# Performance work log

Measured on AMD Instinct MI355X. Metric: run time of the kernel, lower is better.

## Reference

```python
import jax, jax.numpy as jnp
import numpy as np

B, N, D, H, K, MSL = 16, 512, 512, 8, 16, 512
HD = D // H
EPS = 1e-5


def _ln(x, g, b):
    m = jnp.mean(x, axis=-1, keepdims=True)
    v = jnp.mean((x - m) ** 2, axis=-1, keepdims=True)
    return (x - m) * jax.lax.rsqrt(v + EPS) * g + b


def setup_inputs() -> dict:
    key = jax.random.key(0)
    ks = jax.random.split(key, 12)
    s = 0.02
    d = {
        'x': jax.random.normal(ks[0], (B, N, D), jnp.float32),
        'wq': jax.random.normal(ks[1], (D, D), jnp.float32) * s,
        'bq': jnp.zeros((D,), jnp.float32),
        'wk': jax.random.normal(ks[2], (D, D), jnp.float32) * s,
        'bk': jnp.zeros((D,), jnp.float32),
        'wv': jax.random.normal(ks[3], (D, D), jnp.float32) * s,
        'bv': jnp.zeros((D,), jnp.float32),
        'wo': jax.random.normal(ks[4], (D, D), jnp.float32) * s,
        'bo': jnp.zeros((D,), jnp.float32),
        'g1': jnp.ones((D,), jnp.float32),
        'be1': jnp.zeros((D,), jnp.float32),
        'g2': jnp.ones((D,), jnp.float32),
        'be2': jnp.zeros((D,), jnp.float32),
        'w1': jax.random.normal(ks[5], (D, 4 * D), jnp.float32) * s,
        'bf1': jnp.zeros((4 * D,), jnp.float32),
        'w2': jax.random.normal(ks[6], (4 * D, D), jnp.float32) * s,
        'bf2': jnp.zeros((D,), jnp.float32),
        'rel_emb': jax.random.normal(ks[7], (2 * MSL - 1, H), jnp.float32) * s,
    }
    return d


def reference(x, wq, bq, wk, bk, wv, bv, wo, bo, g1, be1, g2, be2, w1, bf1, w2, bf2, rel_emb):
    # Pre-norm attention (dropout = identity, eval mode)
    xn = _ln(x, g1, be1)
    Q = (xn @ wq + bq).reshape(B, N, H, HD)
    Kh = (xn @ wk + bk).reshape(B, N, H, HD)
    V = (xn @ wv + bv).reshape(B, N, H, HD)
    scale = HD ** -0.5
    logits = jnp.einsum('bnhd,bmhd->bhnm', Q, Kh) * scale  # (B,H,N,N)
    # relative temporal bias
    pos = jnp.arange(N)
    drel = pos[None, :] - pos[:, None] + (MSL - 1)  # (N,N)
    bias = rel_emb[drel]  # (N,N,H)
    logits = logits + jnp.transpose(bias, (2, 0, 1))[None]
    # top-k sparsification + softmax over surviving entries only
    vals, idx = jax.lax.top_k(logits, K)  # (B,H,N,K)
    attn_k = jax.nn.softmax(vals, axis=-1)  # softmax over -inf-masked row == softmax over top-k
    # scatter probabilities back into dense (B,H,N,N) rows
    rows = jnp.zeros((B * H * N, N), logits.dtype)
    attn = jax.vmap(lambda r, i, v: r.at[i].set(v))(
        rows, idx.reshape(-1, K), attn_k.reshape(-1, K)
    ).reshape(B, H, N, N)
    out = jnp.einsum('bhnm,bmhd->bnhd', attn, V).reshape(B, N, D)
    out = out @ wo + bo
    x = x + out
    # feed-forward (GELU exact, matching torch default)
    xn2 = _ln(x, g2, be2)
    ff = jax.nn.gelu(xn2 @ w1 + bf1, approximate=False) @ w2 + bf2
    return x + ff
```

## Files before the change

### kernel.cpp

```cpp
#include <hip/hip_runtime.h>
#include <hip/hip_bf16.h>

#define BB 16
#define NN 512
#define DD 512
#define HH 8
#define HD 64
#define MM (BB*NN)
#define DFF 2048

typedef __attribute__((ext_vector_type(8))) short bf16x8;
typedef __attribute__((ext_vector_type(4))) float fx4;

static __device__ __forceinline__ unsigned short f2bf(float f) {
  unsigned u = __float_as_uint(f);
  u += 0x7FFFu + ((u >> 16) & 1u);
  return (unsigned short)(u >> 16);
}
static __device__ __forceinline__ float bf2f(unsigned short s) {
  return __uint_as_float(((unsigned)s) << 16);
}

static __device__ __forceinline__ void load_lds16(const unsigned short* g, unsigned short* l) {
  __builtin_amdgcn_global_load_lds(
      (const __attribute__((address_space(1))) void*)g,
      (__attribute__((address_space(3))) void*)l, 16, 0, 0);
}

__global__ void transpose_all(const float* __restrict__ wq, const float* __restrict__ wk,
                              const float* __restrict__ wv, const float* __restrict__ wo,
                              const float* __restrict__ w1, const float* __restrict__ w2,
                              unsigned short* __restrict__ wqkvT, unsigned short* __restrict__ woT,
                              unsigned short* __restrict__ w1T, unsigned short* __restrict__ w2T) {
  __shared__ float tl[32][33];
  int id = blockIdx.x;
  const float* src; unsigned short* dst; int K, N, bx, by;
  if (id < 1024) {
    int m = id >> 8, tt = id & 255;
    src = (m == 0) ? wq : (m == 1) ? wk : (m == 2) ? wv : wo;
    dst = (m == 3) ? woT : wqkvT + m * 512 * 512;
    K = 512; N = 512; bx = tt & 15; by = tt >> 4;
  } else if (id < 2048) {
    int tt = id - 1024;
    src = w1; dst = w1T; K = 512; N = 2048; bx = tt & 63; by = tt >> 6;
  } else {
    int tt = id - 2048;
    src = w2; dst = w2T; K = 2048; N = 512; bx = tt & 15; by = tt >> 4;
  }
  int tx = threadIdx.x, ty = threadIdx.y;
  int x0 = bx * 32, y0 = by * 32;
  #pragma unroll
  for (int i = 0; i < 4; i++)
    tl[ty + i*8][tx] = src[(size_t)(y0 + ty + i*8) * N + x0 + tx];
  __syncthreads();
  #pragma unroll
  for (int i = 0; i < 4; i++)
    dst[(size_t)(x0 + ty + i*8) * K + y0 + tx] = f2bf(tl[tx][ty + i*8]);
}

__global__ void concat_bias(const float* __restrict__ bq, const float* __restrict__ bk,
                            const float* __restrict__ bv, float* __restrict__ o) {
  int t = blockIdx.x * 256 + threadIdx.x;
  if (t < 512) o[t] = bq[t];
  else if (t < 1024) o[t] = bk[t - 512];
  else if (t < 1536) o[t] = bv[t - 1024];
}

__global__ __launch_bounds__(256) void ln_kernel(const float* __restrict__ X,
                                                 const float* __restrict__ g,
                                                 const float* __restrict__ be,
                                                 unsigned short* __restrict__ O) {
  int w = threadIdx.x >> 6, l = threadIdx.x & 63;
  size_t row = (size_t)blockIdx.x * 4 + w;
  const float* xr = X + row * 512;
  fx4 a = *(const fx4*)(xr + l*4);
  fx4 c = *(const fx4*)(xr + 256 + l*4);
  float s = a[0]+a[1]+a[2]+a[3] + c[0]+c[1]+c[2]+c[3];
  float q = a[0]*a[0]+a[1]*a[1]+a[2]*a[2]+a[3]*a[3]
          + c[0]*c[0]+c[1]*c[1]+c[2]*c[2]+c[3]*c[3];
  #pragma unroll
  for (int s2 = 1; s2 < 64; s2 <<= 1) { s += __shfl_xor(s, s2); q += __shfl_xor(q, s2); }
  float mean = s * (1.0f/512.0f);
  float var  = q * (1.0f/512.0f) - mean*mean;
  float rs = rsqrtf(var + 1e-5f);
  fx4 ga = *(const fx4*)(g + l*4);
  fx4 gc = *(const fx4*)(g + 256 + l*4);
  fx4 ba = *(const fx4*)(be + l*4);
  fx4 bc = *(const fx4*)(be + 256 + l*4);
  ushort4 o1, o2;
  o1.x = f2bf((a[0]-mean)*rs*ga[0] + ba[0]);
  o1.y = f2bf((a[1]-mean)*rs*ga[1] + ba[1]);
  o1.z = f2bf((a[2]-mean)*rs*ga[2] + ba[2]);
  o1.w = f2bf((a[3]-mean)*rs*ga[3] + ba[3]);
  o2.x = f2bf((c[0]-mean)*rs*gc[0] + bc[0]);
  o2.y = f2bf((c[1]-mean)*rs*gc[1] + bc[1]);
  o2.z = f2bf((c[2]-mean)*rs*gc[2] + bc[2]);
  o2.w = f2bf((c[3]-mean)*rs*gc[3] + bc[3]);
  *(ushort4*)(O + row*512 + l*4) = o1;
  *(ushort4*)(O + row*512 + 256 + l*4) = o2;
}

template<int MODE, int TN>
__global__ __launch_bounds__(256) void gemm_kernel(
    const unsigned short* __restrict__ A,
    const unsigned short* __restrict__ Bm,
    const float* __restrict__ bias,
    const float* resid,
    void* C,
    int M, int N, int K) {
  constexpr int MI  = (TN == 128) ? 2 : 1;
  constexpr int BW  = (TN == 128) ? 32 : 16;
  constexpr int NBI = (TN == 128) ? 4 : 2;
  __shared__ unsigned short As[64*64];
  __shared__ unsigned short Bs[TN*64];
  int m0 = blockIdx.y * 64, n0 = blockIdx.x * TN;
  int t = threadIdx.x;
  int w = t >> 6, l = t & 63;
  int wm = (TN == 128) ? (w >> 1) : w;
  int wn = (TN == 128) ? (w & 1) : 0;
  int lid = l & 15, quad = l >> 4;
  int lrow = l >> 3, lch = (l & 7) ^ lrow;

  const unsigned short* gA = A  + (size_t)(m0 + w*16 + lrow)*K + lch*8;
  const unsigned short* gB = Bm + (size_t)(n0 + w*BW + lrow)*K + lch*8;
  unsigned short* lA0 = As + (w*16    )*64;
  unsigned short* lA1 = As + (w*16 + 8)*64;
  unsigned short* lB[NBI];
  #pragma unroll
  for (int i = 0; i < NBI; i++) lB[i] = Bs + (w*BW + i*8)*64;

  fx4 acc[MI][4];
  #pragma unroll
  for (int i = 0; i < MI; i++)
    #pragma unroll
    for (int j = 0; j < 4; j++) acc[i][j] = (fx4){0.f,0.f,0.f,0.f};

  int xA = (lid & 7) * 8;

  for (int k0 = 0; k0 < K; k0 += 64) {
    load_lds16(gA,       lA0);
    load_lds16(gA + 8*K, lA1);
    #pragma unroll
    for (int i = 0; i < NBI; i++) load_lds16(gB + (size_t)(i*8)*K, lB[i]);
    gA += 64; gB += 64;
    __syncthreads();
    #pragma unroll
    for (int s = 0; s < 2; s++) {
      int cbase = (s*4 + quad) * 8;
      bf16x8 af[MI], bf[4];
      #pragma unroll
      for (int i = 0; i < MI; i++) {
        int ra = wm*(MI*16) + i*16 + lid;
        af[i] = *(const bf16x8*)(As + ra*64 + (cbase ^ xA));
      }
      #pragma unroll
      for (int j = 0; j < 4; j++) {
        int rb = wn*64 + j*16 + lid;
        bf[j] = *(const bf16x8*)(Bs + rb*64 + (cbase ^ xA));
      }
      #pragma unroll
      for (int i = 0; i < MI; i++)
        #pragma unroll
        for (int j = 0; j < 4; j++)
          acc[i][j] = __builtin_amdgcn_mfma_f32_16x16x32_bf16(af[i], bf[j], acc[i][j], 0, 0, 0);
    }
    __syncthreads();
  }

  #pragma unroll
  for (int i = 0; i < MI; i++) {
    #pragma unroll
    for (int j = 0; j < 4; j++) {
      int col = n0 + wn*64 + j*16 + lid;
      float bv = bias[col];
      #pragma unroll
      for (int r = 0; r < 4; r++) {
        int row = m0 + wm*(MI*16) + i*16 + quad*4 + r;
        float v = acc[i][j][r] + bv;
        if (MODE == 0) {
          if (col < 512) v *= 0.125f;
          ((unsigned short*)C)[(size_t)row*N + col] = f2bf(v);
        } else if (MODE == 1 || MODE == 3) {
          v += resid[(size_t)row*N + col];
          ((float*)C)[(size_t)row*N + col] = v;
        } else {
          float gl = 0.5f * v * (1.0f + erff(v * 0.70710678118654752f));
          ((unsigned short*)C)[(size_t)row*N + col] = f2bf(gl);
        }
      }
    }
  }
}

__global__ __launch_bounds__(256) void attn_kernel(
    const unsigned short* __restrict__ QKV,
    const float* __restrict__ rel_emb,
    unsigned short* __restrict__ Aout) {
  __shared__ float smem[6144];
  unsigned short* Ks = (unsigned short*)smem;
  float* bias_s = smem + 4608;
  float* pr = smem + 5632;
  int blk = blockIdx.x;
  int q0 = (blk & 7) << 6;
  int bh = blk >> 3;
  int b = bh >> 3, h = bh & 7;
  int t = threadIdx.x;
  int w = t >> 6, l = t & 63;
  int lid = l & 15, quad = l >> 4;

  for (int i = t; i < 1023; i += 256) bias_s[i] = rel_emb[i*8 + h];

  int qn = q0 + w*16 + lid;
  const unsigned short* qp = QKV + ((size_t)(b*512 + qn))*1536 + h*64 + quad*8;
  bf16x8 qf0 = *(const bf16x8*)qp;
  bf16x8 qf1 = *(const bf16x8*)(qp + 32);

  fx4 acc[32];
  #pragma unroll
  for (int i = 0; i < 32; i++) acc[i] = (fx4){0.f,0.f,0.f,0.f};

  #pragma unroll
  for (int chunk = 0; chunk < 4; chunk++) {
    __syncthreads();
    #pragma unroll
    for (int i = 0; i < 4; i++) {
      int c = t + i*256;
      int row = c >> 3, ch = c & 7;
      uint4 d = *(const uint4*)(QKV + ((size_t)(b*512 + chunk*128 + row))*1536 + 512 + h*64 + ch*8);
      *(uint4*)(Ks + row*72 + ch*8) = d;
    }
    __syncthreads();
    #pragma unroll
    for (int kt = 0; kt < 8; kt++) {
      const unsigned short* kp = Ks + (kt*16 + lid)*72 + quad*8;
      bf16x8 kb0 = *(const bf16x8*)kp;
      bf16x8 kb1 = *(const bf16x8*)(kp + 32);
      int ai = chunk*8 + kt;
      acc[ai] = __builtin_amdgcn_mfma_f32_16x16x32_bf16(qf0, kb0, acc[ai], 0, 0, 0);
      acc[ai] = __builtin_amdgcn_mfma_f32_16x16x32_bf16(qf1, kb1, acc[ai], 0, 0, 0);
    }
  }

  int nb = q0 + w*16 + quad*4;
  #pragma unroll
  for (int kt = 0; kt < 32; kt++) {
    int m = kt*16 + lid;
    int bidx = m - nb + 511;
    #pragma unroll
    for (int r = 0; r < 4; r++) {
      float v = acc[kt][r] + bias_s[bidx - r];
      unsigned mu = __float_as_uint(v);
      mu = (mu & 0x80000000u) ? ~mu : (mu | 0x80000000u);
      acc[kt][r] = __uint_as_float((mu & 0xFFFFFE00u) | (unsigned)(511 - m));
    }
  }

  unsigned mx0=0, mx1=0, mx2=0, mx3=0;
  #pragma unroll
  for (int kt = 0; kt < 32; kt++) {
    unsigned u0 = __float_as_uint(acc[kt][0]); mx0 = u0 > mx0 ? u0 : mx0;
    unsigned u1 = __float_as_uint(acc[kt][1]); mx1 = u1 > mx1 ? u1 : mx1;
    unsigned u2 = __float_as_uint(acc[kt][2]); mx2 = u2 > mx2 ? u2 : mx2;
    unsigned u3 = __float_as_uint(acc[kt][3]); mx3 = u3 > mx3 ? u3 : mx3;
  }
  unsigned mn0=mx0, mn1=mx1, mn2=mx2, mn3=mx3;
  #pragma unroll
  for (int s2 = 1; s2 < 16; s2 <<= 1) {
    unsigned o;
    o = __shfl_xor(mn0, s2); mn0 = o < mn0 ? o : mn0;
    o = __shfl_xor(mn1, s2); mn1 = o < mn1 ? o : mn1;
    o = __shfl_xor(mn2, s2); mn2 = o < mn2 ? o : mn2;
    o = __shfl_xor(mn3, s2); mn3 = o < mn3 ? o : mn3;
    o = __shfl_xor(mx0, s2); mx0 = o > mx0 ? o : mx0;
    o = __shfl_xor(mx1, s2); mx1 = o > mx1 ? o : mx1;
    o = __shfl_xor(mx2, s2); mx2 = o > mx2 ? o : mx2;
    o = __shfl_xor(mx3, s2); mx3 = o > mx3 ? o : mx3;
  }
  unsigned lo0 = mn0 - (mn0 ? 1u : 0u), hi0 = mx0;
  unsigned lo1 = mn1 - (mn1 ? 1u : 0u), hi1 = mx1;
  unsigned lo2 = mn2 - (mn2 ? 1u : 0u), hi2 = mx2;
  unsigned lo3 = mn3 - (mn3 ? 1u : 0u), hi3 = mx3;

  unsigned th0=0, th1=0, th2=0, th3=0;
  unsigned done = 0;
  #pragma unroll 1
  for (int it = 0; it < 34; ++it) {
    unsigned d_;
    d_ = hi0-lo0; unsigned mid0 = lo0 + (d_>>1) + (d_&1u);
    d_ = hi1-lo1; unsigned mid1 = lo1 + (d_>>1) + (d_&1u);
    d_ = hi2-lo2; unsigned mid2 = lo2 + (d_>>1) + (d_&1u);
    d_ = hi3-lo3; unsigned mid3 = lo3 + (d_>>1) + (d_&1u);
    unsigned c0=0, c1=0, c2=0, c3=0;
    #pragma unroll
    for (int kt = 0; kt < 32; kt++) {
      c0 += (__float_as_uint(acc[kt][0]) >= mid0);
      c1 += (__float_as_uint(acc[kt][1]) >= mid1);
      c2 += (__float_as_uint(acc[kt][2]) >= mid2);
      c3 += (__float_as_uint(acc[kt][3]) >= mid3);
    }
    unsigned p01 = c0 | (c1 << 16);
    unsigned p23 = c2 | (c3 << 16);
    #pragma unroll
    for (int s2 = 1; s2 < 16; s2 <<= 1) {
      p01 += __shfl_xor(p01, s2);
      p23 += __shfl_xor(p23, s2);
    }
    unsigned C0 = p01 & 0xFFFFu, C1 = p01 >> 16;
    unsigned C2 = p23 & 0xFFFFu, C3 = p23 >> 16;
    { bool f = !(done & 1u); bool e = f && (C0 == 16u);
      th0 = e ? mid0 : th0; done |= e ? 1u : 0u;
      lo0 = (f && C0 > 16u) ? mid0 : lo0; hi0 = (f && C0 < 16u) ? mid0 : hi0; }
    { bool f = !(done & 2u); bool e = f && (C1 == 16u);
      th1 = e ? mid1 : th1; done |= e ? 2u : 0u;
      lo1 = (f && C1 > 16u) ? mid1 : lo1; hi1 = (f && C1 < 16u) ? mid1 : hi1; }
    { bool f = !(done & 4u); bool e = f && (C2 == 16u);
      th2 = e ? mid2 : th2; done |= e ? 4u : 0u;
      lo2 = (f && C2 > 16u) ? mid2 : lo2; hi2 = (f && C2 < 16u) ? mid2 : hi2; }
    { bool f = !(done & 8u); bool e = f && (C3 == 16u);
      th3 = e ? mid3 : th3; done |= e ? 8u : 0u;
      lo3 = (f && C3 > 16u) ? mid3 : lo3; hi3 = (f && C3 < 16u) ? mid3 : hi3; }
    if (__all((int)(done == 15u))) break;
  }

  float* prE = pr + w*128 + quad*32;
  int*   prM = (int*)prE + 16;
  unsigned below = (1u << lid) - 1u;
  #pragma unroll
  for (int r = 0; r < 4; r++) {
    unsigned thr = (r==0) ? th0 : (r==1) ? th1 : (r==2) ? th2 : th3;
    int base = 0;
    #pragma unroll
    for (int kt = 0; kt < 32; kt++) {
      unsigned u = __float_as_uint(acc[kt][r]);
      bool sel = u >= thr;
      unsigned long long bm = __ballot(sel);
      unsigned gm = (unsigned)(bm >> (quad*16)) & 0xFFFFu;
      if (sel) {
        int slot = base + __popc(gm & below);
        unsigned vu = u & 0xFFFFFE00u;
        vu = (vu & 0x80000000u) ? (vu & 0x7FFFFFFFu) : ~vu;
        float e = exp2f(__uint_as_float(vu) * 1.44269504f);
        if (slot < 16) { prE[slot] = e; prM[slot] = 511 - (int)(u & 0x1FFu); }
      }
      base += __popc(gm);
    }
    __threadfence_block();
    int n = nb + r;
    float o0=0.f, o1=0.f, o2=0.f, o3=0.f, es=0.f;
    #pragma unroll
    for (int k2 = 0; k2 < 16; k2++) {
      float e = prE[k2];
      int m = prM[k2];
      const unsigned short* vp = QKV + ((size_t)(b*512 + m))*1536 + 1024 + h*64 + lid*4;
      ushort4 v4 = *(const ushort4*)vp;
      es += e;
      o0 += e * bf2f(v4.x); o1 += e * bf2f(v4.y);
      o2 += e * bf2f(v4.z); o3 += e * bf2f(v4.w);
    }
    float inv = 1.0f / es;
    ushort4 ov;
    ov.x = f2bf(o0*inv); ov.y = f2bf(o1*inv);
    ov.z = f2bf(o2*inv); ov.w = f2bf(o3*inv);
    *(ushort4*)(Aout + ((size_t)(b*512 + n))*512 + h*64 + lid*4) = ov;
    __threadfence_block();
  }
}

extern "C" void kernel_launch(void* const* d_in, const int* in_sizes, int n_in,
                              void* d_out, int out_size, void* d_ws, size_t ws_size,
                              hipStream_t stream) {
  const float* x   = (const float*)d_in[0];
  const float* wq  = (const float*)d_in[1];
  const float* bq  = (const float*)d_in[2];
  const float* wk  = (const float*)d_in[3];
  const float* bk  = (const float*)d_in[4];
  const float* wv  = (const float*)d_in[5];
  const float* bv  = (const float*)d_in[6];
  const float* wo  = (const float*)d_in[7];
  const float* bo  = (const float*)d_in[8];
  const float* g1  = (const float*)d_in[9];
  const float* be1 = (const float*)d_in[10];
  const float* g2  = (const float*)d_in[11];
  const float* be2 = (const float*)d_in[12];
  const float* w1  = (const float*)d_in[13];
  const float* bf1 = (const float*)d_in[14];
  const float* w2  = (const float*)d_in[15];
  const float* bf2 = (const float*)d_in[16];
  const float* rel = (const float*)d_in[17];

  char* p = (char*)d_ws;
  size_t off = 0;
  auto alloc = [&](size_t bytes) {
    size_t cur = off;
    off += (bytes + 255) & ~(size_t)255;
    return (void*)(p + cur);
  };
  unsigned short* wqkvT = (unsigned short*)alloc((size_t)1536*512*2);
  unsigned short* woT   = (unsigned short*)alloc((size_t)512*512*2);
  unsigned short* w1T   = (unsigned short*)alloc((size_t)2048*512*2);
  unsigned short* w2T   = (unsigned short*)alloc((size_t)512*2048*2);
  float*          bqkv  = (float*)alloc(1536*4);
  unsigned short* R1    = (unsigned short*)alloc((size_t)MM*512*2);
  unsigned short* R2    = (unsigned short*)alloc((size_t)MM*2048*2);

  unsigned short* xn1  = R1;
  unsigned short* aout = R1;
  unsigned short* xn2  = R1;
  unsigned short* qkvb = R2;
  unsigned short* hbuf = R2;
  float*          x2   = (float*)d_out;
  (void)ws_size; (void)in_sizes; (void)n_in; (void)out_size;

  transpose_all<<<3072, dim3(32, 8), 0, stream>>>(wq, wk, wv, wo, w1, w2,
                                                  wqkvT, woT, w1T, w2T);
  concat_bias<<<6, 256, 0, stream>>>(bq, bk, bv, bqkv);

  ln_kernel<<<2048, 256, 0, stream>>>(x, g1, be1, xn1);
  gemm_kernel<0,128><<<dim3(12, 128), 256, 0, stream>>>(xn1, wqkvT, bqkv, nullptr, qkvb, MM, 1536, 512);
  attn_kernel<<<1024, 256, 0, stream>>>(qkvb, rel, aout);
  gemm_kernel<1,64><<<dim3(8, 128), 256, 0, stream>>>(aout, woT, bo, x, x2, MM, 512, 512);
  ln_kernel<<<2048, 256, 0, stream>>>(x2, g2, be2, xn2);
  gemm_kernel<2,128><<<dim3(16, 128), 256, 0, stream>>>(xn2, w1T, bf1, nullptr, hbuf, MM, 2048, 512);
  gemm_kernel<3,64><<<dim3(8, 128), 256, 0, stream>>>(hbuf, w2T, bf2, x2, (float*)d_out, MM, 512, 2048);
}
```

Baseline: 347.3 us.

## Double-buffer K tiles via async global-to-LDS loads with XOR swizzle

The attention kernel now stages K chunks into two LDS buffers using direct global-to-LDS loads, prefetching the next chunk while MFMAs consume the current one, which halves the barriers per chunk. The padded layout is replaced by an XOR-swizzled 64-wide layout to avoid bank conflicts without padding. The top-k probability scratch is also double-buffered by row parity so a trailing fence can be dropped. LDS use grows from 24KB to 40KB, which may lower occupancy, and correctness depends on load_lds16 completing before the barrier.

```diff
diff --git a/kernel.cpp b/kernel.cpp
--- a/kernel.cpp
+++ b/kernel.cpp
@@ -196,10 +196,11 @@
     const unsigned short* __restrict__ QKV,
     const float* __restrict__ rel_emb,
     unsigned short* __restrict__ Aout) {
-  __shared__ float smem[6144];
-  unsigned short* Ks = (unsigned short*)smem;
-  float* bias_s = smem + 4608;
-  float* pr = smem + 5632;
+  __shared__ float smem[10240];
+  unsigned short* K0 = (unsigned short*)smem;
+  unsigned short* K1 = (unsigned short*)(smem + 4096);
+  float* bias_s = smem + 8192;
+  float* pr = smem + 9216;
   int blk = blockIdx.x;
   int q0 = (blk & 7) << 6;
   int bh = blk >> 3;
@@ -219,26 +220,34 @@
   #pragma unroll
   for (int i = 0; i < 32; i++) acc[i] = (fx4){0.f,0.f,0.f,0.f};
 
+  int srow = l >> 3, sch = (l & 7) ^ srow;
+  const unsigned short* gK = QKV + ((size_t)(b*512 + w*32 + srow))*1536 + 512 + h*64 + sch*8;
+  unsigned short* lK0 = K0 + w*32*64;
+  unsigned short* lK1 = K1 + w*32*64;
+  #pragma unroll
+  for (int i = 0; i < 4; i++) load_lds16(gK + (size_t)(i*8)*1536, lK0 + i*8*64);
+  __syncthreads();
+
+  int xk = lid & 7;
   #pragma unroll
   for (int chunk = 0; chunk < 4; chunk++) {
-    __syncthreads();
-    #pragma unroll
-    for (int i = 0; i < 4; i++) {
-      int c = t + i*256;
-      int row = c >> 3, ch = c & 7;
-      uint4 d = *(const uint4*)(QKV + ((size_t)(b*512 + chunk*128 + row))*1536 + 512 + h*64 + ch*8);
-      *(uint4*)(Ks + row*72 + ch*8) = d;
-    }
-    __syncthreads();
+    const unsigned short* cur = (chunk & 1) ? K1 : K0;
+    if (chunk < 3) {
+      unsigned short* nxt = (chunk & 1) ? lK0 : lK1;
+      #pragma unroll
+      for (int i = 0; i < 4; i++)
+        load_lds16(gK + (size_t)((chunk+1)*128 + i*8)*1536, nxt + i*8*64);
+    }
     #pragma unroll
     for (int kt = 0; kt < 8; kt++) {
-      const unsigned short* kp = Ks + (kt*16 + lid)*72 + quad*8;
-      bf16x8 kb0 = *(const bf16x8*)kp;
-      bf16x8 kb1 = *(const bf16x8*)(kp + 32);
+      const unsigned short* kp = cur + (kt*16 + lid)*64;
+      bf16x8 kb0 = *(const bf16x8*)(kp + ((quad    ) ^ xk)*8);
+      bf16x8 kb1 = *(const bf16x8*)(kp + ((quad + 4) ^ xk)*8);
       int ai = chunk*8 + kt;
       acc[ai] = __builtin_amdgcn_mfma_f32_16x16x32_bf16(qf0, kb0, acc[ai], 0, 0, 0);
       acc[ai] = __builtin_amdgcn_mfma_f32_16x16x32_bf16(qf1, kb1, acc[ai], 0, 0, 0);
     }
+    if (chunk < 3) __syncthreads();
   }
 
   int nb = q0 + w*16 + quad*4;
@@ -322,11 +331,11 @@
     if (__all((int)(done == 15u))) break;
   }
 
-  float* prE = pr + w*128 + quad*32;
-  int*   prM = (int*)prE + 16;
   unsigned below = (1u << lid) - 1u;
   #pragma unroll
   for (int r = 0; r < 4; r++) {
+    float* prE = pr + (r & 1)*512 + w*128 + quad*32;
+    int*   prM = (int*)prE + 16;
     unsigned thr = (r==0) ? th0 : (r==1) ? th1 : (r==2) ? th2 : th3;
     int base = 0;
     #pragma unroll
@@ -362,7 +371,6 @@
     ov.x = f2bf(o0*inv); ov.y = f2bf(o1*inv);
     ov.z = f2bf(o2*inv); ov.w = f2bf(o3*inv);
     *(ushort4*)(Aout + ((size_t)(b*512 + n))*512 + h*64 + lid*4) = ov;
-    __threadfence_block();
   }
 }
 
```

Result: slower. 408.1 us (+17.5%).

## Swizzle K tile in LDS, use DPP row reductions, double-buffer prob slots

Applied to the files above, without the earlier changes.

The K tile in shared memory moves from padded rows to an XOR-swizzled layout, which removes bank conflicts without the padding. The 16-lane min/max/sum reductions in the top-k threshold search now use DPP row operations instead of shuffles, lowering the latency of each bisection step. The per-row probability/index scratch alternates between two buffers so the trailing block fence can be dropped. Together these trim overhead in the attention kernel, but that kernel is only one part of the whole layer.

```diff
diff --git a/kernel.cpp b/kernel.cpp
--- a/kernel.cpp
+++ b/kernel.cpp
@@ -25,6 +25,30 @@
   __builtin_amdgcn_global_load_lds(
       (const __attribute__((address_space(1))) void*)g,
       (__attribute__((address_space(3))) void*)l, 16, 0, 0);
+}
+
+static __device__ __forceinline__ unsigned dpp_sum16(unsigned v) {
+  v += (unsigned)__builtin_amdgcn_update_dpp(0, (int)v, 0xB1, 0xF, 0xF, false);
+  v += (unsigned)__builtin_amdgcn_update_dpp(0, (int)v, 0x4E, 0xF, 0xF, false);
+  v += (unsigned)__builtin_amdgcn_update_dpp(0, (int)v, 0x124, 0xF, 0xF, false);
+  v += (unsigned)__builtin_amdgcn_update_dpp(0, (int)v, 0x128, 0xF, 0xF, false);
+  return v;
+}
+static __device__ __forceinline__ unsigned dpp_min16(unsigned v) {
+  unsigned o;
+  o = (unsigned)__builtin_amdgcn_update_dpp(0, (int)v, 0xB1, 0xF, 0xF, false);  v = o < v ? o : v;
+  o = (unsigned)__builtin_amdgcn_update_dpp(0, (int)v, 0x4E, 0xF, 0xF, false);  v = o < v ? o : v;
+  o = (unsigned)__builtin_amdgcn_update_dpp(0, (int)v, 0x124, 0xF, 0xF, false); v = o < v ? o : v;
+  o = (unsigned)__builtin_amdgcn_update_dpp(0, (int)v, 0x128, 0xF, 0xF, false); v = o < v ? o : v;
+  return v;
+}
+static __device__ __forceinline__ unsigned dpp_max16(unsigned v) {
+  unsigned o;
+  o = (unsigned)__builtin_amdgcn_update_dpp(0, (int)v, 0xB1, 0xF, 0xF, false);  v = o > v ? o : v;
+  o = (unsigned)__builtin_amdgcn_update_dpp(0, (int)v, 0x4E, 0xF, 0xF, false);  v = o > v ? o : v;
+  o = (unsigned)__builtin_amdgcn_update_dpp(0, (int)v, 0x124, 0xF, 0xF, false); v = o > v ? o : v;
+  o = (unsigned)__builtin_amdgcn_update_dpp(0, (int)v, 0x128, 0xF, 0xF, false); v = o > v ? o : v;
+  return v;
 }
 
 __global__ void transpose_all(const float* __restrict__ wq, const float* __restrict__ wk,
@@ -198,8 +222,8 @@
     unsigned short* __restrict__ Aout) {
   __shared__ float smem[6144];
   unsigned short* Ks = (unsigned short*)smem;
-  float* bias_s = smem + 4608;
-  float* pr = smem + 5632;
+  float* bias_s = smem + 4096;
+  float* pr = smem + 5120;
   int blk = blockIdx.x;
   int q0 = (blk & 7) << 6;
   int bh = blk >> 3;
@@ -219,6 +243,7 @@
   #pragma unroll
   for (int i = 0; i < 32; i++) acc[i] = (fx4){0.f,0.f,0.f,0.f};
 
+  int xk = lid & 7;
   #pragma unroll
   for (int chunk = 0; chunk < 4; chunk++) {
     __syncthreads();
@@ -227,14 +252,14 @@
       int c = t + i*256;
       int row = c >> 3, ch = c & 7;
       uint4 d = *(const uint4*)(QKV + ((size_t)(b*512 + chunk*128 + row))*1536 + 512 + h*64 + ch*8);
-      *(uint4*)(Ks + row*72 + ch*8) = d;
+      *(uint4*)(Ks + row*64 + ((ch ^ (row & 7))*8)) = d;
     }
     __syncthreads();
     #pragma unroll
     for (int kt = 0; kt < 8; kt++) {
-      const unsigned short* kp = Ks + (kt*16 + lid)*72 + quad*8;
-      bf16x8 kb0 = *(const bf16x8*)kp;
-      bf16x8 kb1 = *(const bf16x8*)(kp + 32);
+      const unsigned short* kp = Ks + (kt*16 + lid)*64;
+      bf16x8 kb0 = *(const bf16x8*)(kp + ((quad    ) ^ xk)*8);
+      bf16x8 kb1 = *(const bf16x8*)(kp + ((quad + 4) ^ xk)*8);
       int ai = chunk*8 + kt;
       acc[ai] = __builtin_amdgcn_mfma_f32_16x16x32_bf16(qf0, kb0, acc[ai], 0, 0, 0);
       acc[ai] = __builtin_amdgcn_mfma_f32_16x16x32_bf16(qf1, kb1, acc[ai], 0, 0, 0);
@@ -263,19 +288,10 @@
     unsigned u2 = __float_as_uint(acc[kt][2]); mx2 = u2 > mx2 ? u2 : mx2;
     unsigned u3 = __float_as_uint(acc[kt][3]); mx3 = u3 > mx3 ? u3 : mx3;
   }
-  unsigned mn0=mx0, mn1=mx1, mn2=mx2, mn3=mx3;
-  #pragma unroll
-  for (int s2 = 1; s2 < 16; s2 <<= 1) {
-    unsigned o;
-    o = __shfl_xor(mn0, s2); mn0 = o < mn0 ? o : mn0;
-    o = __shfl_xor(mn1, s2); mn1 = o < mn1 ? o : mn1;
-    o = __shfl_xor(mn2, s2); mn2 = o < mn2 ? o : mn2;
-    o = __shfl_xor(mn3, s2); mn3 = o < mn3 ? o : mn3;
-    o = __shfl_xor(mx0, s2); mx0 = o > mx0 ? o : mx0;
-    o = __shfl_xor(mx1, s2); mx1 = o > mx1 ? o : mx1;
-    o = __shfl_xor(mx2, s2); mx2 = o > mx2 ? o : mx2;
-    o = __shfl_xor(mx3, s2); mx3 = o > mx3 ? o : mx3;
-  }
+  unsigned mn0 = dpp_min16(mx0), mn1 = dpp_min16(mx1);
+  unsigned mn2 = dpp_min16(mx2), mn3 = dpp_min16(mx3);
+  mx0 = dpp_max16(mx0); mx1 = dpp_max16(mx1);
+  mx2 = dpp_max16(mx2); mx3 = dpp_max16(mx3);
   unsigned lo0 = mn0 - (mn0 ? 1u : 0u), hi0 = mx0;
   unsigned lo1 = mn1 - (mn1 ? 1u : 0u), hi1 = mx1;
   unsigned lo2 = mn2 - (mn2 ? 1u : 0u), hi2 = mx2;
@@ -298,13 +314,8 @@
       c2 += (__float_as_uint(acc[kt][2]) >= mid2);
       c3 += (__float_as_uint(acc[kt][3]) >= mid3);
     }
-    unsigned p01 = c0 | (c1 << 16);
-    unsigned p23 = c2 | (c3 << 16);
-    #pragma unroll
-    for (int s2 = 1; s2 < 16; s2 <<= 1) {
-      p01 += __shfl_xor(p01, s2);
-      p23 += __shfl_xor(p23, s2);
-    }
+    unsigned p01 = dpp_sum16(c0 | (c1 << 16));
+    unsigned p23 = dpp_sum16(c2 | (c3 << 16));
     unsigned C0 = p01 & 0xFFFFu, C1 = p01 >> 16;
     unsigned C2 = p23 & 0xFFFFu, C3 = p23 >> 16;
     { bool f = !(done & 1u); bool e = f && (C0 == 16u);
@@ -322,11 +333,11 @@
     if (__all((int)(done == 15u))) break;
   }
 
-  float* prE = pr + w*128 + quad*32;
-  int*   prM = (int*)prE + 16;
   unsigned below = (1u << lid) - 1u;
   #pragma unroll
   for (int r = 0; r < 4; r++) {
+    float* prE = pr + (r & 1)*512 + w*128 + quad*32;
+    int*   prM = (int*)prE + 16;
     unsigned thr = (r==0) ? th0 : (r==1) ? th1 : (r==2) ? th2 : th3;
     int base = 0;
     #pragma unroll
@@ -362,7 +373,6 @@
     ov.x = f2bf(o0*inv); ov.y = f2bf(o1*inv);
     ov.z = f2bf(o2*inv); ov.w = f2bf(o3*inv);
     *(ushort4*)(Aout + ((size_t)(b*512 + n))*512 + h*64 + lid*4) = ov;
-    __threadfence_block();
   }
 }
 
```

After: 385.6 us. 1.11x slower.
